# Performance work log

Hardware: AMD Instinct MI355X
Metric: run time of the kernel (lower is better)

## Reference

```python
import jax, jax.numpy as jnp
import numpy as np

DIM = 768
H = 12
HD = DIM // H  # 64
B = 16
N = 1025  # cls token + 1024 patches; RoPE applied to tokens 1:


def setup_inputs() -> dict:
    key = jax.random.key(0)
    k1, k2, k3, k4, k5, k6 = jax.random.split(key, 6)
    x = jax.random.normal(k1, (B, N, DIM), dtype=jnp.float32)
    # rotary angles for the N-1 non-cls tokens, HD//2 freq pairs
    theta = jax.random.uniform(k2, (N - 1, HD // 2), dtype=jnp.float32) * 2.0 * jnp.pi
    freqs_cos = jnp.cos(theta)
    freqs_sin = jnp.sin(theta)
    W_qkv = jax.random.normal(k3, (3 * DIM, DIM), dtype=jnp.float32) * 0.02
    W_proj = jax.random.normal(k4, (DIM, DIM), dtype=jnp.float32) * 0.02
    b_proj = jax.random.normal(k5, (DIM,), dtype=jnp.float32) * 0.02
    return {"x": x, "freqs_cos": freqs_cos, "freqs_sin": freqs_sin,
            "W_qkv": W_qkv, "W_proj": W_proj, "b_proj": b_proj}


def _apply_rope(t, cos, sin):
    # t: [b, h, m, d]; cos/sin: [m, d/2]. Pairs are interleaved (even, odd),
    # matching torch.view_as_complex on a (..., d/2, 2) reshape.
    tr = t[..., 0::2]
    ti = t[..., 1::2]
    cos = cos[None, None, :, :]
    sin = sin[None, None, :, :]
    out_r = tr * cos - ti * sin
    out_i = tr * sin + ti * cos
    # interleave back: (..., d/2, 2) -> (..., d)
    out = jnp.stack([out_r, out_i], axis=-1)
    return out.reshape(t.shape)


def reference(x, freqs_cos, freqs_sin, W_qkv, W_proj, b_proj):
    b, n, dim = x.shape
    h, hd = H, HD
    scale = hd ** -0.5

    qkv = jnp.einsum('bnd,ed->bne', x, W_qkv)            # [b, n, 3*dim]
    qkv = qkv.reshape(b, n, 3, h, hd)
    q = jnp.transpose(qkv[:, :, 0], (0, 2, 1, 3))         # [b, h, n, hd]
    k = jnp.transpose(qkv[:, :, 1], (0, 2, 1, 3))
    v = jnp.transpose(qkv[:, :, 2], (0, 2, 1, 3))

    # RoPE on all tokens except the cls token (index 0)
    q = jnp.concatenate([q[:, :, :1], _apply_rope(q[:, :, 1:], freqs_cos, freqs_sin)], axis=2)
    k = jnp.concatenate([k[:, :, :1], _apply_rope(k[:, :, 1:], freqs_cos, freqs_sin)], axis=2)

    dots = jnp.einsum('bhid,bhjd->bhij', q, k) * scale    # [b, h, n, n]
    attn = jax.nn.softmax(dots, axis=-1)
    out = jnp.einsum('bhij,bhjd->bhid', attn, v)          # [b, h, n, hd]
    out = jnp.transpose(out, (0, 2, 1, 3)).reshape(b, n, dim)
    out = jnp.einsum('bnd,ed->bne', out, W_proj) + b_proj
    return out
```

## Files before the change

### kernel.cpp

```cpp
#include <hip/hip_runtime.h>
#include <stdint.h>

#define NH 12
#define HD64 64
#define SEQ 1025
#define M_ROWS (16 * SEQ)
#define DIM 768
#define NPAD 1088

typedef __attribute__((ext_vector_type(8))) short bf16x8;
typedef __attribute__((ext_vector_type(4))) float f32x4;
typedef __attribute__((ext_vector_type(4))) short s16x4;

#define VMCNT(n) asm volatile("s_waitcnt vmcnt(" #n ")" ::: "memory")
#define LGKMCNT0 asm volatile("s_waitcnt lgkmcnt(0)" ::: "memory")

__device__ __forceinline__ short f2bf_rne(float f) {
    union { float f; uint32_t u; } c; c.f = f;
    uint32_t u = c.u + 0x7fffu + ((c.u >> 16) & 1u);
    return (short)(u >> 16);
}

__device__ __forceinline__ int cvt_pk_bf16(float lo, float hi) {
    int r;
    asm("v_cvt_pk_bf16_f32 %0, %1, %2" : "=v"(r) : "v"(lo), "v"(hi));
    return r;
}

__device__ __forceinline__ void gload_lds16(const void* g, void* l) {
    __builtin_amdgcn_global_load_lds(
        (const __attribute__((address_space(1))) void*)g,
        (__attribute__((address_space(3))) void*)l, 16, 0, 0);
}

__device__ __forceinline__ int xcd_chunk_swizzle(int orig, int nwg) {
    int q = nwg >> 3, r = nwg & 7;
    int xcd = orig & 7, i = orig >> 3;
    int start = (xcd < r) ? xcd * (q + 1) : r * (q + 1) + (xcd - r) * q;
    return start + i;
}

__global__ void f2bf_kernel(const float* __restrict__ in, short* __restrict__ out, int n4) {
    int i = blockIdx.x * blockDim.x + threadIdx.x;
    if (i < n4) {
        f32x4 f = ((const f32x4*)in)[i];
        s16x4 o;
        o[0] = f2bf_rne(f[0]); o[1] = f2bf_rne(f[1]);
        o[2] = f2bf_rne(f[2]); o[3] = f2bf_rne(f[3]);
        ((s16x4*)out)[i] = o;
    }
}

__global__ __launch_bounds__(256) void qkv_gemm_kernel(
    const short* __restrict__ xb, const short* __restrict__ wb,
    const float* __restrict__ fcos, const float* __restrict__ fsin,
    short* __restrict__ Qb, short* __restrict__ Kb, short* __restrict__ VTb)
{
    __shared__ short Alds[3][128 * 32];
    __shared__ short Blds[3][128 * 32];
    const int tid = threadIdx.x;
    const int lane = tid & 63, w = tid >> 6;
    const int wm = w >> 1, wn = w & 1;
    const int lr = lane & 15, lg = lane >> 4;
    const int tile = xcd_chunk_swizzle(blockIdx.x, 129 * 18);
    const int mt = tile / 18, nt = tile - (tile / 18) * 18;

    const int c0 = tid, c1 = 256 + tid;
    int ra0 = mt * 128 + (c0 >> 2); if (ra0 > M_ROWS - 1) ra0 = M_ROWS - 1;
    int ra1 = mt * 128 + (c1 >> 2); if (ra1 > M_ROWS - 1) ra1 = M_ROWS - 1;
    const short* gA0 = xb + (size_t)ra0 * DIM + (c0 & 3) * 8;
    const short* gA1 = xb + (size_t)ra1 * DIM + (c1 & 3) * 8;
    const short* gB0 = wb + (size_t)(nt * 128 + (c0 >> 2)) * DIM + (c0 & 3) * 8;
    const short* gB1 = wb + (size_t)(nt * 128 + (c1 >> 2)) * DIM + (c1 & 3) * 8;
    short* lA0 = &Alds[0][0] + c0 * 8;
    short* lA1 = &Alds[0][0] + c1 * 8;
    short* lB0 = &Blds[0][0] + c0 * 8;
    short* lB1 = &Blds[0][0] + c1 * 8;

    auto stage = [&](int buf, int kt) {
        const int ko = kt * 32;
        const int lo = buf * (128 * 32);
        gload_lds16(gA0 + ko, lA0 + lo);
        gload_lds16(gA1 + ko, lA1 + lo);
        gload_lds16(gB0 + ko, lB0 + lo);
        gload_lds16(gB1 + ko, lB1 + lo);
    };

    f32x4 acc[4][4];
#pragma unroll
    for (int i = 0; i < 4; i++)
#pragma unroll
        for (int j = 0; j < 4; j++) acc[i][j] = (f32x4)0.0f;

    stage(0, 0); stage(1, 1); stage(2, 2);

    int cur = 0;
    for (int t = 0; t < 24; ++t) {
        if (t <= 21) { VMCNT(8); } else if (t == 22) { VMCNT(4); } else { VMCNT(0); }
        __builtin_amdgcn_s_barrier();

        bf16x8 af[4], bfr[4];
        const short* Ab = &Alds[0][0] + cur * (128 * 32);
        const short* Bb = &Blds[0][0] + cur * (128 * 32);
#pragma unroll
        for (int mi = 0; mi < 4; mi++)
            af[mi] = *(const bf16x8*)&Ab[(wm * 64 + mi * 16 + lr) * 32 + lg * 8];
#pragma unroll
        for (int ni = 0; ni < 4; ni++)
            bfr[ni] = *(const bf16x8*)&Bb[(wn * 64 + ni * 16 + lr) * 32 + lg * 8];

        if (t <= 20) {
            LGKMCNT0;
            __builtin_amdgcn_s_barrier();
            stage(cur, t + 3);
        }

#pragma unroll
        for (int mi = 0; mi < 4; mi++)
#pragma unroll
            for (int ni = 0; ni < 4; ni++)
                acc[mi][ni] = __builtin_amdgcn_mfma_f32_16x16x32_bf16(af[mi], bfr[ni], acc[mi][ni], 0, 0, 0);

        cur = (cur == 2) ? 0 : cur + 1;
    }

#pragma unroll
    for (int mi = 0; mi < 4; mi++) {
        int mbase = mt * 128 + wm * 64 + mi * 16 + lg * 4;
#pragma unroll
        for (int j = 0; j < 4; j++) {
            int m = mbase + j;
            bool valid = (m < M_ROWS);
            int mm = valid ? m : 0;
            int b = mm / SEQ;
            int n = mm - b * SEQ;
#pragma unroll
            for (int ni = 0; ni < 4; ni++) {
                int e = nt * 128 + wn * 64 + ni * 16 + lr;
                int qkv = e / DIM;
                int rem = e - qkv * DIM;
                int h = rem >> 6, d = rem & 63;
                float v = acc[mi][ni][j];
                float vo = __shfl_xor(v, 1);
                float outv = v;
                if (qkv < 2 && n > 0) {
                    float cs = fcos[(n - 1) * 32 + (d >> 1)];
                    float sn = fsin[(n - 1) * 32 + (d >> 1)];
                    outv = (d & 1) ? (vo * sn + v * cs) : (v * cs - vo * sn);
                }
                if (qkv == 0) outv *= 0.180336881f;
                if (valid) {
                    short bv = f2bf_rne(outv);
                    size_t bh = (size_t)b * NH + h;
                    if (qkv == 0)      Qb[(bh * SEQ + n) * HD64 + d] = bv;
                    else if (qkv == 1) Kb[(bh * SEQ + n) * HD64 + d] = bv;
                    else               VTb[(bh * HD64 + d) * NPAD + n] = bv;
                }
            }
        }
    }
}

__global__ __launch_bounds__(256) void attn_kernel(
    const short* __restrict__ Qb, const short* __restrict__ Kb,
    const short* __restrict__ VTb, short* __restrict__ AO)
{
    __shared__ short Klds[2][64 * 64];
    __shared__ short Vlds[2][64 * 64];
    __shared__ int Plds[4][16 * 32];
    const int tid = threadIdx.x;
    const int lane = tid & 63, w = tid >> 6;
    const int lr = lane & 15, lg = lane >> 4;
    const int tile = xcd_chunk_swizzle(blockIdx.x, 17 * 192);
    const int bh = tile / 17, qt = tile - (tile / 17) * 17;
    const int b = bh / NH, h = bh - b * NH;

    const short* Qp = Qb + (size_t)bh * SEQ * HD64;
    const short* Kp = Kb + (size_t)bh * SEQ * HD64;
    const short* Vp = VTb + (size_t)bh * HD64 * NPAD;

    int qr = qt * 64 + w * 16 + lr; if (qr > SEQ - 1) qr = SEQ - 1;
    bf16x8 qf0 = *(const bf16x8*)&Qp[(size_t)qr * HD64 + 0 + lg * 8];
    bf16x8 qf1 = *(const bf16x8*)&Qp[(size_t)qr * HD64 + 32 + lg * 8];

    float m_i = -1e30f, l_i = 0.f;
    f32x4 acc[4];
#pragma unroll
    for (int vt = 0; vt < 4; vt++) acc[vt] = (f32x4)0.0f;

    int* pw = &Plds[w][0];
    const int pswz = (lr & 3) << 3;

    auto stageKV = [&](int buf, int t) {
        int k0 = t * 64;
#pragma unroll
        for (int i = 0; i < 2; i++) {
            int c = i * 256 + tid;
            int row = c >> 3, ccd = c & 7;
            int cl = ccd ^ (row & 7);
            int krow = k0 + row; if (krow > SEQ - 1) krow = SEQ - 1;
            gload_lds16(Kp + (size_t)krow * HD64 + cl * 8, &Klds[buf][c * 8]);
            gload_lds16(Vp + (size_t)row * NPAD + k0 + cl * 8, &Vlds[buf][c * 8]);
        }
    };

    stageKV(0, 0);
    asm volatile("s_waitcnt vmcnt(0)" ::: "memory");
    __syncthreads();

    for (int t = 0; t < 17; ++t) {
        int cur = t & 1;
        if (t < 16) stageKV(cur ^ 1, t + 1);

        f32x4 s[4];
#pragma unroll
        for (int k16 = 0; k16 < 4; k16++) {
            int krow = k16 * 16 + lr;
            bf16x8 kf0 = *(const bf16x8*)&Klds[cur][krow * 64 + ((0 + lg) ^ (krow & 7)) * 8];
            bf16x8 kf1 = *(const bf16x8*)&Klds[cur][krow * 64 + ((4 + lg) ^ (krow & 7)) * 8];
            f32x4 d = (f32x4)0.0f;
            d = __builtin_amdgcn_mfma_f32_16x16x32_bf16(kf0, qf0, d, 0, 0, 0);
            d = __builtin_amdgcn_mfma_f32_16x16x32_bf16(kf1, qf1, d, 0, 0, 0);
            s[k16] = d;
        }
        if (t == 16) {
            s[0][0] = (lg == 0) ? s[0][0] : -1e30f;
            s[0][1] = -1e30f; s[0][2] = -1e30f; s[0][3] = -1e30f;
#pragma unroll
            for (int k16 = 1; k16 < 4; k16++) { s[k16][0] = -1e30f; s[k16][1] = -1e30f; s[k16][2] = -1e30f; s[k16][3] = -1e30f; }
        }

        float a0 = fmaxf(s[0][0], s[0][1]), a1 = fmaxf(s[0][2], s[0][3]);
        float a2 = fmaxf(s[1][0], s[1][1]), a3 = fmaxf(s[1][2], s[1][3]);
        float a4 = fmaxf(s[2][0], s[2][1]), a5 = fmaxf(s[2][2], s[2][3]);
        float a6 = fmaxf(s[3][0], s[3][1]), a7 = fmaxf(s[3][2], s[3][3]);
        float b0 = fmaxf(fmaxf(a0, a1), fmaxf(a2, a3));
        float b1 = fmaxf(fmaxf(a4, a5), fmaxf(a6, a7));
        float pmax = fmaxf(b0, b1);
        pmax = fmaxf(pmax, __shfl_xor(pmax, 16));
        pmax = fmaxf(pmax, __shfl_xor(pmax, 32));

        if (__any(pmax > m_i + 11.54f)) {
            float mnew = fmaxf(m_i, pmax);
            float sc = exp2f(m_i - mnew);
            m_i = mnew;
            l_i *= sc;
#pragma unroll
            for (int j = 0; j < 4; j++) {
                float scj = __shfl(sc, 4 * lg + j);
#pragma unroll
                for (int vt = 0; vt < 4; vt++) acc[vt][j] *= scj;
            }
        }

#pragma unroll
        for (int k16 = 0; k16 < 4; k16++) {
#pragma unroll
            for (int j = 0; j < 4; j++) s[k16][j] = exp2f(s[k16][j] - m_i);
        }
        float r0 = (s[0][0] + s[0][1]) + (s[0][2] + s[0][3]);
        float r1 = (s[1][0] + s[1][1]) + (s[1][2] + s[1][3]);
        float r2 = (s[2][0] + s[2][1]) + (s[2][2] + s[2][3]);
        float r3 = (s[3][0] + s[3][1]) + (s[3][2] + s[3][3]);
        float rowsum = (r0 + r1) + (r2 + r3);
        rowsum += __shfl_xor(rowsum, 16);
        rowsum += __shfl_xor(rowsum, 32);
        l_i += rowsum;

#pragma unroll
        for (int k16 = 0; k16 < 4; k16++) {
            int pk0 = cvt_pk_bf16(s[k16][0], s[k16][1]);
            int pk1 = cvt_pk_bf16(s[k16][2], s[k16][3]);
            int pbase = 8 * k16 + 2 * lg;
            pw[lr * 32 + ((pbase + 0) ^ pswz)] = pk0;
            pw[lr * 32 + ((pbase + 1) ^ pswz)] = pk1;
        }
        bf16x8 pa0 = *(const bf16x8*)&pw[lr * 32 + ((4 * lg) ^ pswz)];
        bf16x8 pa1 = *(const bf16x8*)&pw[lr * 32 + ((16 + 4 * lg) ^ pswz)];

#pragma unroll
        for (int vt = 0; vt < 4; vt++) {
            int dr = vt * 16 + lr;
            bf16x8 vf0 = *(const bf16x8*)&Vlds[cur][dr * 64 + ((0 + lg) ^ (dr & 7)) * 8];
            bf16x8 vf1 = *(const bf16x8*)&Vlds[cur][dr * 64 + ((4 + lg) ^ (dr & 7)) * 8];
            acc[vt] = __builtin_amdgcn_mfma_f32_16x16x32_bf16(pa0, vf0, acc[vt], 0, 0, 0);
            acc[vt] = __builtin_amdgcn_mfma_f32_16x16x32_bf16(pa1, vf1, acc[vt], 0, 0, 0);
        }

        asm volatile("s_waitcnt vmcnt(0)" ::: "memory");
        __syncthreads();
    }

    float inv[4];
#pragma unroll
    for (int j = 0; j < 4; j++) inv[j] = 1.0f / __shfl(l_i, 4 * lg + j);
#pragma unroll
    for (int vt = 0; vt < 4; vt++) {
#pragma unroll
        for (int j = 0; j < 4; j++) {
            int qrow = qt * 64 + w * 16 + lg * 4 + j;
            if (qrow < SEQ) {
                AO[((size_t)(b * SEQ + qrow)) * DIM + h * HD64 + vt * 16 + lr] =
                    f2bf_rne(acc[vt][j] * inv[j]);
            }
        }
    }
}

__global__ __launch_bounds__(256) void proj_gemm_kernel(
    const short* __restrict__ ab, const short* __restrict__ wb,
    const float* __restrict__ bias, float* __restrict__ out)
{
    __shared__ short Alds[3][128 * 32];
    __shared__ short Blds[3][128 * 32];
    const int tid = threadIdx.x;
    const int lane = tid & 63, w = tid >> 6;
    const int wm = w >> 1, wn = w & 1;
    const int lr = lane & 15, lg = lane >> 4;
    const int tile = xcd_chunk_swizzle(blockIdx.x, 129 * 6);
    const int mt = tile / 6, nt = tile - (tile / 6) * 6;

    const int c0 = tid, c1 = 256 + tid;
    int ra0 = mt * 128 + (c0 >> 2); if (ra0 > M_ROWS - 1) ra0 = M_ROWS - 1;
    int ra1 = mt * 128 + (c1 >> 2); if (ra1 > M_ROWS - 1) ra1 = M_ROWS - 1;
    const short* gA0 = ab + (size_t)ra0 * DIM + (c0 & 3) * 8;
    const short* gA1 = ab + (size_t)ra1 * DIM + (c1 & 3) * 8;
    const short* gB0 = wb + (size_t)(nt * 128 + (c0 >> 2)) * DIM + (c0 & 3) * 8;
    const short* gB1 = wb + (size_t)(nt * 128 + (c1 >> 2)) * DIM + (c1 & 3) * 8;
    short* lA0 = &Alds[0][0] + c0 * 8;
    short* lA1 = &Alds[0][0] + c1 * 8;
    short* lB0 = &Blds[0][0] + c0 * 8;
    short* lB1 = &Blds[0][0] + c1 * 8;

    auto stage = [&](int buf, int kt) {
        const int ko = kt * 32;
        const int lo = buf * (128 * 32);
        gload_lds16(gA0 + ko, lA0 + lo);
        gload_lds16(gA1 + ko, lA1 + lo);
        gload_lds16(gB0 + ko, lB0 + lo);
        gload_lds16(gB1 + ko, lB1 + lo);
    };

    f32x4 acc[4][4];
#pragma unroll
    for (int i = 0; i < 4; i++)
#pragma unroll
        for (int j = 0; j < 4; j++) acc[i][j] = (f32x4)0.0f;

    stage(0, 0); stage(1, 1); stage(2, 2);

    int cur = 0;
    for (int t = 0; t < 24; ++t) {
        if (t <= 21) { VMCNT(8); } else if (t == 22) { VMCNT(4); } else { VMCNT(0); }
        __builtin_amdgcn_s_barrier();

        bf16x8 af[4], bfr[4];
        const short* Ab = &Alds[0][0] + cur * (128 * 32);
        const short* Bb = &Blds[0][0] + cur * (128 * 32);
#pragma unroll
        for (int mi = 0; mi < 4; mi++)
            af[mi] = *(const bf16x8*)&Ab[(wm * 64 + mi * 16 + lr) * 32 + lg * 8];
#pragma unroll
        for (int ni = 0; ni < 4; ni++)
            bfr[ni] = *(const bf16x8*)&Bb[(wn * 64 + ni * 16 + lr) * 32 + lg * 8];

        if (t <= 20) {
            LGKMCNT0;
            __builtin_amdgcn_s_barrier();
            stage(cur, t + 3);
        }

#pragma unroll
        for (int mi = 0; mi < 4; mi++)
#pragma unroll
            for (int ni = 0; ni < 4; ni++)
                acc[mi][ni] = __builtin_amdgcn_mfma_f32_16x16x32_bf16(af[mi], bfr[ni], acc[mi][ni], 0, 0, 0);

        cur = (cur == 2) ? 0 : cur + 1;
    }

#pragma unroll
    for (int ni = 0; ni < 4; ni++) {
        int e = nt * 128 + wn * 64 + ni * 16 + lr;
        float bv = bias[e];
#pragma unroll
        for (int mi = 0; mi < 4; mi++) {
#pragma unroll
            for (int j = 0; j < 4; j++) {
                int m = mt * 128 + wm * 64 + mi * 16 + lg * 4 + j;
                if (m < M_ROWS) out[(size_t)m * DIM + e] = acc[mi][ni][j] + bv;
            }
        }
    }
}

extern "C" void kernel_launch(void* const* d_in, const int* in_sizes, int n_in,
                              void* d_out, int out_size, void* d_ws, size_t ws_size,
                              hipStream_t stream) {
    const float* x     = (const float*)d_in[0];
    const float* fcos  = (const float*)d_in[1];
    const float* fsin  = (const float*)d_in[2];
    const float* wqkv  = (const float*)d_in[3];
    const float* wproj = (const float*)d_in[4];
    const float* bproj = (const float*)d_in[5];
    float* out = (float*)d_out;

    char* ws = (char*)d_ws;
    size_t off = 0;
    auto salloc = [&](size_t bytes) { void* p = ws + off; off += (bytes + 255) & ~(size_t)255; return p; };
    short* xb     = (short*)salloc((size_t)M_ROWS * DIM * 2);
    short* wqkvb  = (short*)salloc((size_t)2304 * DIM * 2);
    short* wprojb = (short*)salloc((size_t)DIM * DIM * 2);
    short* Qb     = (short*)salloc((size_t)192 * SEQ * HD64 * 2);
    short* Kb     = (short*)salloc((size_t)192 * SEQ * HD64 * 2);
    short* VTb    = (short*)salloc((size_t)192 * HD64 * NPAD * 2);
    short* AO     = (short*)salloc((size_t)M_ROWS * DIM * 2);

    {
        int n4 = M_ROWS * DIM / 4;
        f2bf_kernel<<<(n4 + 255) / 256, 256, 0, stream>>>(x, xb, n4);
    }
    {
        int n4 = 2304 * DIM / 4;
        f2bf_kernel<<<(n4 + 255) / 256, 256, 0, stream>>>(wqkv, wqkvb, n4);
    }
    {
        int n4 = DIM * DIM / 4;
        f2bf_kernel<<<(n4 + 255) / 256, 256, 0, stream>>>(wproj, wprojb, n4);
    }

    qkv_gemm_kernel<<<129 * 18, 256, 0, stream>>>(xb, wqkvb, fcos, fsin, Qb, Kb, VTb);
    attn_kernel<<<17 * 192, 256, 0, stream>>>(Qb, Kb, VTb, AO);
    proj_gemm_kernel<<<129 * 6, 256, 0, stream>>>(AO, wprojb, bproj, out);
}
```

Measured before the change: 336.4 us.

## Enlarge GEMM tiles to 256x256 with 4-stage LDS ring and swizzle

Both GEMMs move from 128x128 tiles on 256 threads to 256x256 tiles on 512 threads, roughly doubling data reuse per LDS load. They use a 4-deep LDS ring, which removes the second barrier and lgkmcnt wait per k-step, and an XOR swizzle on LDS groups to cut bank conflicts. MFMA sections in the GEMMs and in attention get raised wave priority, and the three fp32-to-bf16 conversions merge into one launch. The risks are fewer blocks: the projection GEMM drops to 195 blocks, fewer than the CU count. The larger tiles also raise register and LDS pressure, using 128KB of shared memory per block.

After: 379.2 us. +12.7%, slower.

```diff
diff --git a/kernel.cpp b/kernel.cpp
--- a/kernel.cpp
+++ b/kernel.cpp
@@ -13,7 +13,6 @@
 typedef __attribute__((ext_vector_type(4))) short s16x4;
 
 #define VMCNT(n) asm volatile("s_waitcnt vmcnt(" #n ")" ::: "memory")
-#define LGKMCNT0 asm volatile("s_waitcnt lgkmcnt(0)" ::: "memory")
 
 __device__ __forceinline__ short f2bf_rne(float f) {
     union { float f; uint32_t u; } c; c.f = f;
@@ -40,38 +39,46 @@
     return start + i;
 }
 
-__global__ void f2bf_kernel(const float* __restrict__ in, short* __restrict__ out, int n4) {
+__global__ void f2bf3_kernel(const float* __restrict__ a, short* __restrict__ ao, int na4,
+                             const float* __restrict__ b, short* __restrict__ bo, int nb4,
+                             const float* __restrict__ c, short* __restrict__ co, int nc4) {
     int i = blockIdx.x * blockDim.x + threadIdx.x;
-    if (i < n4) {
-        f32x4 f = ((const f32x4*)in)[i];
-        s16x4 o;
-        o[0] = f2bf_rne(f[0]); o[1] = f2bf_rne(f[1]);
-        o[2] = f2bf_rne(f[2]); o[3] = f2bf_rne(f[3]);
-        ((s16x4*)out)[i] = o;
-    }
-}
-
-__global__ __launch_bounds__(256) void qkv_gemm_kernel(
+    const float* src; short* dst; int idx;
+    if (i < na4) { src = a; dst = ao; idx = i; }
+    else if (i < na4 + nb4) { src = b; dst = bo; idx = i - na4; }
+    else if (i < na4 + nb4 + nc4) { src = c; dst = co; idx = i - na4 - nb4; }
+    else return;
+    f32x4 f = ((const f32x4*)src)[idx];
+    s16x4 o;
+    o[0] = f2bf_rne(f[0]); o[1] = f2bf_rne(f[1]);
+    o[2] = f2bf_rne(f[2]); o[3] = f2bf_rne(f[3]);
+    ((s16x4*)dst)[idx] = o;
+}
+
+
+__global__ __launch_bounds__(512) void qkv_gemm_kernel(
     const short* __restrict__ xb, const short* __restrict__ wb,
     const float* __restrict__ fcos, const float* __restrict__ fsin,
     short* __restrict__ Qb, short* __restrict__ Kb, short* __restrict__ VTb)
 {
-    __shared__ short Alds[3][128 * 32];
-    __shared__ short Blds[3][128 * 32];
+    __shared__ short Alds[4][256 * 32];
+    __shared__ short Blds[4][256 * 32];
     const int tid = threadIdx.x;
     const int lane = tid & 63, w = tid >> 6;
-    const int wm = w >> 1, wn = w & 1;
+    const int wm = w >> 2, wn = w & 3;
     const int lr = lane & 15, lg = lane >> 4;
-    const int tile = xcd_chunk_swizzle(blockIdx.x, 129 * 18);
-    const int mt = tile / 18, nt = tile - (tile / 18) * 18;
-
-    const int c0 = tid, c1 = 256 + tid;
-    int ra0 = mt * 128 + (c0 >> 2); if (ra0 > M_ROWS - 1) ra0 = M_ROWS - 1;
-    int ra1 = mt * 128 + (c1 >> 2); if (ra1 > M_ROWS - 1) ra1 = M_ROWS - 1;
-    const short* gA0 = xb + (size_t)ra0 * DIM + (c0 & 3) * 8;
-    const short* gA1 = xb + (size_t)ra1 * DIM + (c1 & 3) * 8;
-    const short* gB0 = wb + (size_t)(nt * 128 + (c0 >> 2)) * DIM + (c0 & 3) * 8;
-    const short* gB1 = wb + (size_t)(nt * 128 + (c1 >> 2)) * DIM + (c1 & 3) * 8;
+    const int tile = xcd_chunk_swizzle(blockIdx.x, 65 * 9);
+    const int mt = tile / 9, nt = tile - (tile / 9) * 9;
+
+    const int c0 = tid, c1 = tid + 512;
+    int ra0 = mt * 256 + (c0 >> 2); if (ra0 > M_ROWS - 1) ra0 = M_ROWS - 1;
+    int ra1 = mt * 256 + (c1 >> 2); if (ra1 > M_ROWS - 1) ra1 = M_ROWS - 1;
+    const int g0 = (c0 & 3) ^ ((c0 >> 2) & 3) ^ ((c0 >> 4) & 1);
+    const int g1 = (c1 & 3) ^ ((c1 >> 2) & 3) ^ ((c1 >> 4) & 1);
+    const short* gA0 = xb + (size_t)ra0 * DIM + g0 * 8;
+    const short* gA1 = xb + (size_t)ra1 * DIM + g1 * 8;
+    const short* gB0 = wb + (size_t)(nt * 256 + (c0 >> 2)) * DIM + g0 * 8;
+    const short* gB1 = wb + (size_t)(nt * 256 + (c1 >> 2)) * DIM + g1 * 8;
     short* lA0 = &Alds[0][0] + c0 * 8;
     short* lA1 = &Alds[0][0] + c1 * 8;
     short* lB0 = &Blds[0][0] + c0 * 8;
@@ -79,54 +86,52 @@
 
     auto stage = [&](int buf, int kt) {
         const int ko = kt * 32;
-        const int lo = buf * (128 * 32);
+        const int lo = buf * (256 * 32);
         gload_lds16(gA0 + ko, lA0 + lo);
         gload_lds16(gA1 + ko, lA1 + lo);
         gload_lds16(gB0 + ko, lB0 + lo);
         gload_lds16(gB1 + ko, lB1 + lo);
     };
 
-    f32x4 acc[4][4];
-#pragma unroll
-    for (int i = 0; i < 4; i++)
+    f32x4 acc[8][4];
+#pragma unroll
+    for (int i = 0; i < 8; i++)
 #pragma unroll
         for (int j = 0; j < 4; j++) acc[i][j] = (f32x4)0.0f;
 
     stage(0, 0); stage(1, 1); stage(2, 2);
 
-    int cur = 0;
+    const int ablk = (lg ^ (lr & 3) ^ ((lr >> 2) & 1)) * 8;
+
     for (int t = 0; t < 24; ++t) {
-        if (t <= 21) { VMCNT(8); } else if (t == 22) { VMCNT(4); } else { VMCNT(0); }
+        if (t < 22) { VMCNT(8); } else if (t == 22) { VMCNT(4); } else { VMCNT(0); }
         __builtin_amdgcn_s_barrier();
 
-        bf16x8 af[4], bfr[4];
-        const short* Ab = &Alds[0][0] + cur * (128 * 32);
-        const short* Bb = &Blds[0][0] + cur * (128 * 32);
-#pragma unroll
-        for (int mi = 0; mi < 4; mi++)
-            af[mi] = *(const bf16x8*)&Ab[(wm * 64 + mi * 16 + lr) * 32 + lg * 8];
+        const short* Ab = &Alds[0][0] + (t & 3) * (256 * 32);
+        const short* Bb = &Blds[0][0] + (t & 3) * (256 * 32);
+
+        if (t < 21) stage((t + 3) & 3, t + 3);
+
+        bf16x8 bF[4], aF[8];
 #pragma unroll
         for (int ni = 0; ni < 4; ni++)
-            bfr[ni] = *(const bf16x8*)&Bb[(wn * 64 + ni * 16 + lr) * 32 + lg * 8];
-
-        if (t <= 20) {
-            LGKMCNT0;
-            __builtin_amdgcn_s_barrier();
-            stage(cur, t + 3);
-        }
-
-#pragma unroll
-        for (int mi = 0; mi < 4; mi++)
+            bF[ni] = *(const bf16x8*)&Bb[(wn * 64 + ni * 16 + lr) * 32 + ablk];
+#pragma unroll
+        for (int mi = 0; mi < 8; mi++)
+            aF[mi] = *(const bf16x8*)&Ab[(wm * 128 + mi * 16 + lr) * 32 + ablk];
+
+        __builtin_amdgcn_s_setprio(1);
+#pragma unroll
+        for (int mi = 0; mi < 8; mi++)
 #pragma unroll
             for (int ni = 0; ni < 4; ni++)
-                acc[mi][ni] = __builtin_amdgcn_mfma_f32_16x16x32_bf16(af[mi], bfr[ni], acc[mi][ni], 0, 0, 0);
-
-        cur = (cur == 2) ? 0 : cur + 1;
-    }
-
-#pragma unroll
-    for (int mi = 0; mi < 4; mi++) {
-        int mbase = mt * 128 + wm * 64 + mi * 16 + lg * 4;
+                acc[mi][ni] = __builtin_amdgcn_mfma_f32_16x16x32_bf16(aF[mi], bF[ni], acc[mi][ni], 0, 0, 0);
+        __builtin_amdgcn_s_setprio(0);
+    }
+
+#pragma unroll
+    for (int mi = 0; mi < 8; mi++) {
+        int mbase = mt * 256 + wm * 128 + mi * 16 + lg * 4;
 #pragma unroll
         for (int j = 0; j < 4; j++) {
             int m = mbase + j;
@@ -136,7 +141,7 @@
             int n = mm - b * SEQ;
 #pragma unroll
             for (int ni = 0; ni < 4; ni++) {
-                int e = nt * 128 + wn * 64 + ni * 16 + lr;
+                int e = nt * 256 + wn * 64 + ni * 16 + lr;
                 int qkv = e / DIM;
                 int rem = e - qkv * DIM;
                 int h = rem >> 6, d = rem & 63;
@@ -213,6 +218,7 @@
         if (t < 16) stageKV(cur ^ 1, t + 1);
 
         f32x4 s[4];
+        __builtin_amdgcn_s_setprio(1);
 #pragma unroll
         for (int k16 = 0; k16 < 4; k16++) {
             int krow = k16 * 16 + lr;
@@ -223,6 +229,7 @@
             d = __builtin_amdgcn_mfma_f32_16x16x32_bf16(kf1, qf1, d, 0, 0, 0);
             s[k16] = d;
         }
+        __builtin_amdgcn_s_setprio(0);
         if (t == 16) {
             s[0][0] = (lg == 0) ? s[0][0] : -1e30f;
             s[0][1] = -1e30f; s[0][2] = -1e30f; s[0][3] = -1e30f;
@@ -278,6 +285,7 @@
         bf16x8 pa0 = *(const bf16x8*)&pw[lr * 32 + ((4 * lg) ^ pswz)];
         bf16x8 pa1 = *(const bf16x8*)&pw[lr * 32 + ((16 + 4 * lg) ^ pswz)];
 
+        __builtin_amdgcn_s_setprio(1);
 #pragma unroll
         for (int vt = 0; vt < 4; vt++) {
             int dr = vt * 16 + lr;
@@ -286,6 +294,7 @@
             acc[vt] = __builtin_amdgcn_mfma_f32_16x16x32_bf16(pa0, vf0, acc[vt], 0, 0, 0);
             acc[vt] = __builtin_amdgcn_mfma_f32_16x16x32_bf16(pa1, vf1, acc[vt], 0, 0, 0);
         }
+        __builtin_amdgcn_s_setprio(0);
 
         asm volatile("s_waitcnt vmcnt(0)" ::: "memory");
         __syncthreads();
@@ -307,26 +316,28 @@
     }
 }
 
-__global__ __launch_bounds__(256) void proj_gemm_kernel(
+__global__ __launch_bounds__(512) void proj_gemm_kernel(
     const short* __restrict__ ab, const short* __restrict__ wb,
     const float* __restrict__ bias, float* __restrict__ out)
 {
-    __shared__ short Alds[3][128 * 32];
-    __shared__ short Blds[3][128 * 32];
+    __shared__ short Alds[4][256 * 32];
+    __shared__ short Blds[4][256 * 32];
     const int tid = threadIdx.x;
     const int lane = tid & 63, w = tid >> 6;
-    const int wm = w >> 1, wn = w & 1;
+    const int wm = w >> 2, wn = w & 3;
     const int lr = lane & 15, lg = lane >> 4;
-    const int tile = xcd_chunk_swizzle(blockIdx.x, 129 * 6);
-    const int mt = tile / 6, nt = tile - (tile / 6) * 6;
-
-    const int c0 = tid, c1 = 256 + tid;
-    int ra0 = mt * 128 + (c0 >> 2); if (ra0 > M_ROWS - 1) ra0 = M_ROWS - 1;
-    int ra1 = mt * 128 + (c1 >> 2); if (ra1 > M_ROWS - 1) ra1 = M_ROWS - 1;
-    const short* gA0 = ab + (size_t)ra0 * DIM + (c0 & 3) * 8;
-    const short* gA1 = ab + (size_t)ra1 * DIM + (c1 & 3) * 8;
-    const short* gB0 = wb + (size_t)(nt * 128 + (c0 >> 2)) * DIM + (c0 & 3) * 8;
-    const short* gB1 = wb + (size_t)(nt * 128 + (c1 >> 2)) * DIM + (c1 & 3) * 8;
+    const int tile = xcd_chunk_swizzle(blockIdx.x, 65 * 3);
+    const int mt = tile / 3, nt = tile - (tile / 3) * 3;
+
+    const int c0 = tid, c1 = tid + 512;
+    int ra0 = mt * 256 + (c0 >> 2); if (ra0 > M_ROWS - 1) ra0 = M_ROWS - 1;
+    int ra1 = mt * 256 + (c1 >> 2); if (ra1 > M_ROWS - 1) ra1 = M_ROWS - 1;
+    const int g0 = (c0 & 3) ^ ((c0 >> 2) & 3) ^ ((c0 >> 4) & 1);
+    const int g1 = (c1 & 3) ^ ((c1 >> 2) & 3) ^ ((c1 >> 4) & 1);
+    const short* gA0 = ab + (size_t)ra0 * DIM + g0 * 8;
+    const short* gA1 = ab + (size_t)ra1 * DIM + g1 * 8;
+    const short* gB0 = wb + (size_t)(nt * 256 + (c0 >> 2)) * DIM + g0 * 8;
+    const short* gB1 = wb + (size_t)(nt * 256 + (c1 >> 2)) * DIM + g1 * 8;
     short* lA0 = &Alds[0][0] + c0 * 8;
     short* lA1 = &Alds[0][0] + c1 * 8;
     short* lB0 = &Blds[0][0] + c0 * 8;
@@ -334,60 +345,58 @@
 
     auto stage = [&](int buf, int kt) {
         const int ko = kt * 32;
-        const int lo = buf * (128 * 32);
+        const int lo = buf * (256 * 32);
         gload_lds16(gA0 + ko, lA0 + lo);
         gload_lds16(gA1 + ko, lA1 + lo);
         gload_lds16(gB0 + ko, lB0 + lo);
         gload_lds16(gB1 + ko, lB1 + lo);
     };
 
-    f32x4 acc[4][4];
-#pragma unroll
-    for (int i = 0; i < 4; i++)
+    f32x4 acc[8][4];
+#pragma unroll
+    for (int i = 0; i < 8; i++)
 #pragma unroll
         for (int j = 0; j < 4; j++) acc[i][j] = (f32x4)0.0f;
 
     stage(0, 0); stage(1, 1); stage(2, 2);
 
-    int cur = 0;
+    const int ablk = (lg ^ (lr & 3) ^ ((lr >> 2) & 1)) * 8;
+
     for (int t = 0; t < 24; ++t) {
-        if (t <= 21) { VMCNT(8); } else if (t == 22) { VMCNT(4); } else { VMCNT(0); }
+        if (t < 22) { VMCNT(8); } else if (t == 22) { VMCNT(4); } else { VMCNT(0); }
         __builtin_amdgcn_s_barrier();
 
-        bf16x8 af[4], bfr[4];
-        const short* Ab = &Alds[0][0] + cur * (128 * 32);
-        const short* Bb = &Blds[0][0] + cur * (128 * 32);
-#pragma unroll
-        for (int mi = 0; mi < 4; mi++)
-            af[mi] = *(const bf16x8*)&Ab[(wm * 64 + mi * 16 + lr) * 32 + lg * 8];
+        const short* Ab = &Alds[0][0] + (t & 3) * (256 * 32);
+        const short* Bb = &Blds[0][0] + (t & 3) * (256 * 32);
+
+        if (t < 21) stage((t + 3) & 3, t + 3);
+
+        bf16x8 bF[4], aF[8];
 #pragma unroll
         for (int ni = 0; ni < 4; ni++)
-            bfr[ni] = *(const bf16x8*)&Bb[(wn * 64 + ni * 16 + lr) * 32 + lg * 8];
-
-        if (t <= 20) {
-            LGKMCNT0;
-            __builtin_amdgcn_s_barrier();
-            stage(cur, t + 3);
-        }
-
-#pragma unroll
-        for (int mi = 0; mi < 4; mi++)
+            bF[ni] = *(const bf16x8*)&Bb[(wn * 64 + ni * 16 + lr) * 32 + ablk];
+#pragma unroll
+        for (int mi = 0; mi < 8; mi++)
+            aF[mi] = *(const bf16x8*)&Ab[(wm * 128 + mi * 16 + lr) * 32 + ablk];
+
+        __builtin_amdgcn_s_setprio(1);
+#pragma unroll
+        for (int mi = 0; mi < 8; mi++)
 #pragma unroll
             for (int ni = 0; ni < 4; ni++)
-                acc[mi][ni] = __builtin_amdgcn_mfma_f32_16x16x32_bf16(af[mi], bfr[ni], acc[mi][ni], 0, 0, 0);
-
-        cur = (cur == 2) ? 0 : cur + 1;
+                acc[mi][ni] = __builtin_amdgcn_mfma_f32_16x16x32_bf16(aF[mi], bF[ni], acc[mi][ni], 0, 0, 0);
+        __builtin_amdgcn_s_setprio(0);
     }
 
 #pragma unroll
     for (int ni = 0; ni < 4; ni++) {
-        int e = nt * 128 + wn * 64 + ni * 16 + lr;
+        int e = nt * 256 + wn * 64 + ni * 16 + lr;
         float bv = bias[e];
 #pragma unroll
-        for (int mi = 0; mi < 4; mi++) {
+        for (int mi = 0; mi < 8; mi++) {
 #pragma unroll
             for (int j = 0; j < 4; j++) {
-                int m = mt * 128 + wm * 64 + mi * 16 + lg * 4 + j;
+                int m = mt * 256 + wm * 128 + mi * 16 + lg * 4 + j;
                 if (m < M_ROWS) out[(size_t)m * DIM + e] = acc[mi][ni][j] + bv;
             }
         }
@@ -417,19 +426,14 @@
     short* AO     = (short*)salloc((size_t)M_ROWS * DIM * 2);
 
     {
-        int n4 = M_ROWS * DIM / 4;
-        f2bf_kernel<<<(n4 + 255) / 256, 256, 0, stream>>>(x, xb, n4);
-    }
-    {
-        int n4 = 2304 * DIM / 4;
-        f2bf_kernel<<<(n4 + 255) / 256, 256, 0, stream>>>(wqkv, wqkvb, n4);
-    }
-    {
-        int n4 = DIM * DIM / 4;
-        f2bf_kernel<<<(n4 + 255) / 256, 256, 0, stream>>>(wproj, wprojb, n4);
-    }
-
-    qkv_gemm_kernel<<<129 * 18, 256, 0, stream>>>(xb, wqkvb, fcos, fsin, Qb, Kb, VTb);
+        int na4 = M_ROWS * DIM / 4;
+        int nb4 = 2304 * DIM / 4;
+        int nc4 = DIM * DIM / 4;
+        int tot = na4 + nb4 + nc4;
+        f2bf3_kernel<<<(tot + 255) / 256, 256, 0, stream>>>(x, xb, na4, wqkv, wqkvb, nb4, wproj, wprojb, nc4);
+    }
+
+    qkv_gemm_kernel<<<65 * 9, 512, 0, stream>>>(xb, wqkvb, fcos, fsin, Qb, Kb, VTb);
     attn_kernel<<<17 * 192, 256, 0, stream>>>(Qb, Kb, VTb, AO);
-    proj_gemm_kernel<<<129 * 6, 256, 0, stream>>>(AO, wprojb, bproj, out);
-}
+    proj_gemm_kernel<<<65 * 3, 512, 0, stream>>>(AO, wprojb, bproj, out);
+}
```
